# Kernel tuning notes

Measured on AMD Instinct MI355X. Metric: run time of the kernel, lower is better.

Reference implementation:

```python
import math
import jax, jax.numpy as jnp
import numpy as np


def setup_inputs() -> dict:
    key = jax.random.key(0)
    ks = jax.random.split(key, 8)
    N, Lv, M, Lt = 4096, 16, 4096, 77
    Din, D, R = 512, 768, 4  # fc in-dim, model dim, bottleneck ratio
    Dh = D // R
    s = lambda k, shape, fan_in: jax.random.normal(k, shape, jnp.float32) * (1.0 / math.sqrt(fan_in))
    return {
        "vision_prompt": jax.random.normal(ks[0], (N, Lv, D), jnp.float32),
        "text_prompt": jax.random.normal(ks[1], (M, Lt, Din), jnp.float32),
        "fc_w": s(ks[2], (D, Din), Din),        # torch Linear layout [out, in]
        "fc_b": jnp.zeros((D,), jnp.float32),
        "ln_g": jnp.ones((D,), jnp.float32),
        "ln_b": jnp.zeros((D,), jnp.float32),
        "mlp_w1": s(ks[3], (Dh, D), D),
        "mlp_b1": jnp.zeros((Dh,), jnp.float32),
        "mlp_w2": s(ks[4], (D, Dh), Dh),
        "mlp_b2": jnp.zeros((D,), jnp.float32),
    }


def _layernorm(x, g, b, eps=1e-5):
    mu = jnp.mean(x, axis=-1, keepdims=True)
    var = jnp.var(x, axis=-1, keepdims=True)
    return (x - mu) * jax.lax.rsqrt(var + eps) * g + b


def reference(vision_prompt, text_prompt, fc_w, fc_b, ln_g, ln_b,
              mlp_w1, mlp_b1, mlp_w2, mlp_b2):
    N, Lv, D = vision_prompt.shape
    mean_v = jnp.mean(vision_prompt, axis=1)                    # [N, D]
    mean_t = jnp.mean(text_prompt, axis=1)                      # [M, Din]
    t = mean_t @ fc_w.T + fc_b                                  # [M, D]
    scores = jnp.einsum('nc,mc->nm', mean_v, t) / math.sqrt(D)  # [N, M]
    aff = jax.nn.softmax(scores, axis=-1)
    agg = jnp.einsum('nm,mc->nc', aff, t)                       # [N, D]
    h = _layernorm(agg, ln_g, ln_b)
    h = jax.nn.relu(h @ mlp_w1.T + mlp_b1)
    h = h @ mlp_w2.T + mlp_b2                                   # [N, D]
    return jnp.broadcast_to(h[:, None, :], (N, Lv, D))
```

## Files before the change

kernel.cpp:

```cpp
#include <hip/hip_runtime.h>
#include <math.h>

typedef unsigned short u16;
typedef __attribute__((ext_vector_type(4))) float f32x4;
typedef __attribute__((ext_vector_type(8))) short bf16x8;

#define GLOBAL_AS __attribute__((address_space(1)))
#define LDS_AS __attribute__((address_space(3)))

__device__ __forceinline__ u16 f2bf(float f) {
  unsigned u = __builtin_bit_cast(unsigned, f);
  unsigned lsb = (u >> 16) & 1u;
  u += 0x7fffu + lsb;
  return (u16)(u >> 16);
}

__device__ __forceinline__ float bf2f(u16 b) {
  return __builtin_bit_cast(float, ((unsigned)b) << 16);
}

__device__ __forceinline__ void gload16(const void* g, void* l) {
  __builtin_amdgcn_global_load_lds((const GLOBAL_AS void*)g, (LDS_AS void*)l, 16, 0, 0);
}

__global__ __launch_bounds__(256) void prologue_kernel(
    const float* __restrict__ vision, const float* __restrict__ text,
    const float* __restrict__ fc_w, const float* __restrict__ w1,
    const float* __restrict__ w2, const float* __restrict__ b1,
    u16* __restrict__ mean_v, u16* __restrict__ mean_t,
    u16* __restrict__ fcw_bf, u16* __restrict__ w1p, u16* __restrict__ w2p,
    float* __restrict__ b1p)
{
  const int n_mv = 4096 * 192;
  const int n_mt = 4096 * 128;
  const int n_fcw = 768 * 512;
  const int n_w1 = 256 * 768;
  const int n_w2 = 768 * 256;
  int id = blockIdx.x * 256 + threadIdx.x;

  if (id < n_mv) {
    int n = id / 192, c = id % 192;
    const f32x4* x = (const f32x4*)vision + (size_t)n * 16 * 192 + c;
    f32x4 s = {0.f, 0.f, 0.f, 0.f};
#pragma unroll
    for (int l = 0; l < 16; ++l) s += x[(size_t)l * 192];
    s *= (1.f / 16.f);
    ushort4 o; o.x = f2bf(s.x); o.y = f2bf(s.y); o.z = f2bf(s.z); o.w = f2bf(s.w);
    ((ushort4*)mean_v)[id] = o;
    return;
  }
  id -= n_mv;
  if (id < n_mt) {
    int n = id / 128, c = id % 128;
    const f32x4* x = (const f32x4*)text + (size_t)n * 77 * 128 + c;
    f32x4 s = {0.f, 0.f, 0.f, 0.f};
    for (int l = 0; l < 77; ++l) s += x[(size_t)l * 128];
    s *= (1.f / 77.f);
    ushort4 o; o.x = f2bf(s.x); o.y = f2bf(s.y); o.z = f2bf(s.z); o.w = f2bf(s.w);
    ((ushort4*)mean_t)[id] = o;
    return;
  }
  id -= n_mt;
  if (id < n_fcw) { fcw_bf[id] = f2bf(fc_w[id]); return; }
  id -= n_fcw;
  if (id < n_w1) {
    int r = id / 768;
    w1p[id] = (r < 192) ? f2bf(w1[id]) : (u16)0;
    return;
  }
  id -= n_w1;
  if (id < n_w2) {
    int r = id / 256, c = id % 256;
    w2p[id] = (c < 192) ? f2bf(w2[(size_t)r * 192 + c]) : (u16)0;
    return;
  }
  id -= n_w2;
  if (id < 256) b1p[id] = (id < 192) ? b1[id] : 0.f;
}

template<bool EXP>
__global__ __launch_bounds__(512, 2) void gemm256_nt_bf16(
    const u16* __restrict__ A, const u16* __restrict__ B, float alpha,
    u16* __restrict__ C, int N, int K, int lda, int ldb)
{
  __shared__ u16 lA[3][256 * 32];
  __shared__ u16 lB[3][256 * 32];
  const int tid = threadIdx.x;
  const int w = tid >> 6, lane = tid & 63;
  const int brow = blockIdx.y * 256, bcol = blockIdx.x * 256;
  const int wr = w >> 2, wc = w & 3;

  f32x4 acc[8][4];
#pragma unroll
  for (int i = 0; i < 8; ++i)
#pragma unroll
    for (int j = 0; j < 4; ++j) acc[i][j] = (f32x4){0.f, 0.f, 0.f, 0.f};

  const int srow = lane >> 2;
  const int scol = (lane & 3) * 8;
  const size_t ga0 = (size_t)(brow + (w * 2 + 0) * 16 + srow) * lda + scol;
  const size_t ga1 = (size_t)(brow + (w * 2 + 1) * 16 + srow) * lda + scol;
  const size_t gb0 = (size_t)(bcol + (w * 2 + 0) * 16 + srow) * ldb + scol;
  const size_t gb1 = (size_t)(bcol + (w * 2 + 1) * 16 + srow) * ldb + scol;

  const int fr = lane & 15, fk = (lane >> 4) * 8;
  const int NT = K >> 5;

  auto stage = [&](int ti, int b) {
    const int k0 = ti << 5;
    char* la = (char*)&lA[b][0] + w * 2048;
    char* lb = (char*)&lB[b][0] + w * 2048;
    gload16(A + ga0 + k0, la);
    gload16(A + ga1 + k0, la + 1024);
    gload16(B + gb0 + k0, lb);
    gload16(B + gb1 + k0, lb + 1024);
  };

  stage(0, 0);
  stage(1, 1);

  int bR = 0;
  for (int it = 0; it < NT; ++it) {
    if (it + 1 < NT) { asm volatile("s_waitcnt vmcnt(4)" ::: "memory"); }
    else             { asm volatile("s_waitcnt vmcnt(0)" ::: "memory"); }
    __builtin_amdgcn_s_barrier();
    asm volatile("" ::: "memory");

    int bW = bR + 2; if (bW >= 3) bW -= 3;
    if (it + 2 < NT) stage(it + 2, bW);

    const u16* la = lA[bR];
    const u16* lb = lB[bR];
    bf16x8 av[8], bv[4];
#pragma unroll
    for (int mi = 0; mi < 8; ++mi)
      av[mi] = *(const bf16x8*)&la[(wr * 128 + mi * 16 + fr) * 32 + fk];
#pragma unroll
    for (int ni = 0; ni < 4; ++ni)
      bv[ni] = *(const bf16x8*)&lb[(wc * 64 + ni * 16 + fr) * 32 + fk];

    __builtin_amdgcn_s_setprio(1);
#pragma unroll
    for (int mi = 0; mi < 8; ++mi)
#pragma unroll
      for (int ni = 0; ni < 4; ++ni)
        acc[mi][ni] = __builtin_amdgcn_mfma_f32_16x16x32_bf16(av[mi], bv[ni], acc[mi][ni], 0, 0, 0);
    __builtin_amdgcn_s_setprio(0);

    bR = (bR + 1 == 3) ? 0 : bR + 1;
  }

  const int fq = lane >> 4;
#pragma unroll
  for (int mi = 0; mi < 8; ++mi) {
#pragma unroll
    for (int ni = 0; ni < 4; ++ni) {
      int col = bcol + wc * 64 + ni * 16 + fr;
#pragma unroll
      for (int r = 0; r < 4; ++r) {
        int row = brow + wr * 128 + mi * 16 + fq * 4 + r;
        float v = acc[mi][ni][r] * alpha;
        if (EXP) v = __expf(v);
        C[(size_t)row * N + col] = f2bf(v);
      }
    }
  }
}

template<bool RELU, bool BF16OUT>
__global__ __launch_bounds__(256) void gemm_nt(
    const u16* __restrict__ A, const u16* __restrict__ B,
    const float* __restrict__ bias, float alpha,
    float* __restrict__ Cf, u16* __restrict__ Cb,
    int M, int N, int K, int lda, int ldb,
    int kofs, long long cofs)
{
  __shared__ u16 lA[3][128 * 32];
  __shared__ u16 lB[3][128 * 32];
  const int t = threadIdx.x;
  const int w = t >> 6, lane = t & 63;
  const int brow = blockIdx.y * 128, bcol = blockIdx.x * 128;
  const int wr = w >> 1, wc = w & 1;
  const int kz = blockIdx.z;

  A += (size_t)kz * kofs;
  B += (size_t)kz * kofs;
  Cf += kz * cofs;

  f32x4 acc[4][4];
#pragma unroll
  for (int i = 0; i < 4; ++i)
#pragma unroll
    for (int j = 0; j < 4; ++j) acc[i][j] = (f32x4){0.f, 0.f, 0.f, 0.f};

  const int srow = t >> 2;
  const int scol = (t & 3) * 8;
  const size_t aoff0 = (size_t)(brow + srow) * lda + scol;
  const size_t boff0 = (size_t)(bcol + srow) * ldb + scol;
  const size_t aoff1 = aoff0 + (size_t)64 * lda;
  const size_t boff1 = boff0 + (size_t)64 * ldb;

  const int fr = lane & 15, fk = (lane >> 4) * 8;
  const int NT = K >> 5;

  auto stage = [&](int ti, int b) {
    const int k0 = ti << 5;
    char* la = (char*)&lA[b][0] + w * 1024;
    char* lb = (char*)&lB[b][0] + w * 1024;
    gload16(A + aoff0 + k0, la);
    gload16(A + aoff1 + k0, la + 4096);
    gload16(B + boff0 + k0, lb);
    gload16(B + boff1 + k0, lb + 4096);
  };

  stage(0, 0);
  stage(1, 1);

  int bR = 0;
  for (int it = 0; it < NT; ++it) {
    if (it + 1 < NT) { asm volatile("s_waitcnt vmcnt(4)" ::: "memory"); }
    else             { asm volatile("s_waitcnt vmcnt(0)" ::: "memory"); }
    __builtin_amdgcn_s_barrier();
    asm volatile("" ::: "memory");

    int bW = bR + 2; if (bW >= 3) bW -= 3;
    if (it + 2 < NT) stage(it + 2, bW);

    const u16* la = lA[bR];
    const u16* lb = lB[bR];
    bf16x8 av[4], bv[4];
#pragma unroll
    for (int mi = 0; mi < 4; ++mi)
      av[mi] = *(const bf16x8*)&la[(wr * 64 + mi * 16 + fr) * 32 + fk];
#pragma unroll
    for (int ni = 0; ni < 4; ++ni)
      bv[ni] = *(const bf16x8*)&lb[(wc * 64 + ni * 16 + fr) * 32 + fk];

    __builtin_amdgcn_s_setprio(1);
#pragma unroll
    for (int mi = 0; mi < 4; ++mi)
#pragma unroll
      for (int ni = 0; ni < 4; ++ni)
        acc[mi][ni] = __builtin_amdgcn_mfma_f32_16x16x32_bf16(av[mi], bv[ni], acc[mi][ni], 0, 0, 0);
    __builtin_amdgcn_s_setprio(0);

    bR = (bR + 1 == 3) ? 0 : bR + 1;
  }

  const int fq = lane >> 4;
#pragma unroll
  for (int mi = 0; mi < 4; ++mi) {
#pragma unroll
    for (int ni = 0; ni < 4; ++ni) {
      int col = bcol + wc * 64 + ni * 16 + fr;
      float bb = bias ? bias[col] : 0.f;
#pragma unroll
      for (int r = 0; r < 4; ++r) {
        int row = brow + wr * 64 + mi * 16 + fq * 4 + r;
        float v = acc[mi][ni][r] * alpha + bb;
        if (RELU) v = fmaxf(v, 0.f);
        if (BF16OUT) Cb[(size_t)row * N + col] = f2bf(v);
        else         Cf[(size_t)row * N + col] = v;
      }
    }
  }
}

__global__ __launch_bounds__(256) void transpose_bf16_kernel(
    const u16* __restrict__ X, u16* __restrict__ Y, int R, int C)
{
  __shared__ u16 tile[32][33];
  int bx = blockIdx.x, by = blockIdx.y;
  int tx = threadIdx.x & 31, ty = threadIdx.x >> 5;
#pragma unroll
  for (int i = 0; i < 4; ++i) {
    int r = by * 32 + ty + i * 8, c = bx * 32 + tx;
    tile[ty + i * 8][tx] = X[(size_t)r * C + c];
  }
  __syncthreads();
#pragma unroll
  for (int i = 0; i < 4; ++i) {
    int r = bx * 32 + ty + i * 8;
    int c = by * 32 + tx;
    Y[(size_t)r * R + c] = tile[tx][ty + i * 8];
  }
}

__global__ __launch_bounds__(256) void rowsum_kernel(
    const u16* __restrict__ A, float* __restrict__ denom)
{
  __shared__ float red[4];
  int row = blockIdx.x, t = threadIdx.x;
  const u16* s = A + (size_t)row * 4096;
  bf16x8 c0 = *(const bf16x8*)&s[t * 8];
  bf16x8 c1 = *(const bf16x8*)&s[2048 + t * 8];
  float sum = 0.f;
#pragma unroll
  for (int j = 0; j < 8; ++j) sum += bf2f((u16)c0[j]) + bf2f((u16)c1[j]);
#pragma unroll
  for (int off = 32; off > 0; off >>= 1) sum += __shfl_xor(sum, off);
  if ((t & 63) == 0) red[t >> 6] = sum;
  __syncthreads();
  if (t == 0) denom[row] = red[0] + red[1] + red[2] + red[3];
}

__global__ __launch_bounds__(256) void ln4_kernel(
    const float* __restrict__ X, long long ps, const float* __restrict__ denom,
    const float* __restrict__ g, const float* __restrict__ b,
    u16* __restrict__ Y)
{
  __shared__ float red[4];
  int row = blockIdx.x, t = threadIdx.x;
  const float* x = X + (size_t)row * 768;
  float inv_d = 1.f / denom[row];
  float v0 = (x[t]       + x[ps + t]       + x[2 * ps + t]       + x[3 * ps + t]) * inv_d;
  float v1 = (x[t + 256] + x[ps + t + 256] + x[2 * ps + t + 256] + x[3 * ps + t + 256]) * inv_d;
  float v2 = (x[t + 512] + x[ps + t + 512] + x[2 * ps + t + 512] + x[3 * ps + t + 512]) * inv_d;

  float s = v0 + v1 + v2;
#pragma unroll
  for (int off = 32; off > 0; off >>= 1) s += __shfl_xor(s, off);
  if ((t & 63) == 0) red[t >> 6] = s;
  __syncthreads();
  float mu = (red[0] + red[1] + red[2] + red[3]) * (1.f / 768.f);
  __syncthreads();

  float d0 = v0 - mu, d1 = v1 - mu, d2 = v2 - mu;
  float q = d0 * d0 + d1 * d1 + d2 * d2;
#pragma unroll
  for (int off = 32; off > 0; off >>= 1) q += __shfl_xor(q, off);
  if ((t & 63) == 0) red[t >> 6] = q;
  __syncthreads();
  float var = (red[0] + red[1] + red[2] + red[3]) * (1.f / 768.f);
  float inv = rsqrtf(var + 1e-5f);

  u16* y = Y + (size_t)row * 768;
  y[t]       = f2bf(d0 * inv * g[t]       + b[t]);
  y[t + 256] = f2bf(d1 * inv * g[t + 256] + b[t + 256]);
  y[t + 512] = f2bf(d2 * inv * g[t + 512] + b[t + 512]);
}

__global__ __launch_bounds__(256) void bcast_kernel(
    const f32x4* __restrict__ H, f32x4* __restrict__ O, int total, int L, int d4)
{
  int id = blockIdx.x * 256 + threadIdx.x;
  if (id >= total) return;
  int n = id / (L * d4);
  int c = id % d4;
  O[id] = H[(size_t)n * d4 + c];
}

extern "C" void kernel_launch(void* const* d_in, const int* in_sizes, int n_in,
                              void* d_out, int out_size, void* d_ws, size_t ws_size,
                              hipStream_t stream)
{
  const float* vision = (const float*)d_in[0];
  const float* text   = (const float*)d_in[1];
  const float* fc_w   = (const float*)d_in[2];
  const float* fc_b   = (const float*)d_in[3];
  const float* ln_g   = (const float*)d_in[4];
  const float* ln_b   = (const float*)d_in[5];
  const float* w1     = (const float*)d_in[6];
  const float* b1     = (const float*)d_in[7];
  const float* w2     = (const float*)d_in[8];
  const float* b2     = (const float*)d_in[9];
  float* out = (float*)d_out;

  const int N = 4096, Lv = 16, M = 4096, Din = 512, D = 768, Dhp = 256;

  char* p = (char*)d_ws;
  auto alloc = [&](size_t bytes) { char* r = p; p += (bytes + 255) & ~(size_t)255; return r; };
  u16*   mean_v = (u16*)alloc((size_t)N * D * 2);
  u16*   mean_t = (u16*)alloc((size_t)M * Din * 2);
  u16*   fcw_bf = (u16*)alloc((size_t)D * Din * 2);
  u16*   w1p    = (u16*)alloc((size_t)Dhp * D * 2);
  u16*   w2p    = (u16*)alloc((size_t)D * Dhp * 2);
  float* b1p    = (float*)alloc((size_t)Dhp * 4);
  float* denom  = (float*)alloc((size_t)N * 4);
  u16*   t_bf   = (u16*)alloc((size_t)M * D * 2);
  u16*   tT_bf  = (u16*)alloc((size_t)D * M * 2);
  u16*   aff    = (u16*)alloc((size_t)N * M * 2);
  u16*   ln_o   = (u16*)alloc((size_t)N * D * 2);
  u16*   h1     = (u16*)alloc((size_t)N * Dhp * 2);
  float* aggp   = (float*)alloc((size_t)4 * N * D * 4);
  float* h2     = (float*)aff;

  {
    int total = 4096 * 192 + 4096 * 128 + 768 * 512 + 256 * 768 + 768 * 256 + 256;
    prologue_kernel<<<(total + 255) / 256, 256, 0, stream>>>(
        vision, text, fc_w, w1, w2, b1, mean_v, mean_t, fcw_bf, w1p, w2p, b1p);
  }

  gemm_nt<false, true><<<dim3(D / 128, M / 128), 256, 0, stream>>>(
      mean_t, fcw_bf, fc_b, 1.f, nullptr, t_bf, M, D, Din, Din, Din, 0, 0);

  transpose_bf16_kernel<<<dim3(D / 32, M / 32), 256, 0, stream>>>(t_bf, tT_bf, M, D);

  gemm256_nt_bf16<true><<<dim3(M / 256, N / 256), 512, 0, stream>>>(
      mean_v, t_bf, 1.f / sqrtf(768.f), aff, M, D, D, D);

  rowsum_kernel<<<N, 256, 0, stream>>>(aff, denom);

  gemm_nt<false, false><<<dim3(D / 128, N / 128, 4), 256, 0, stream>>>(
      aff, tT_bf, nullptr, 1.f, aggp, nullptr, N, D, M / 4, M, M,
      M / 4, (long long)N * D);

  ln4_kernel<<<N, 256, 0, stream>>>(aggp, (long long)N * D, denom, ln_g, ln_b, ln_o);

  gemm_nt<true, true><<<dim3(Dhp / 128, N / 128), 256, 0, stream>>>(
      ln_o, w1p, b1p, 1.f, nullptr, h1, N, Dhp, D, D, D, 0, 0);

  gemm_nt<false, false><<<dim3(D / 128, N / 128), 256, 0, stream>>>(
      h1, w2p, b2, 1.f, h2, nullptr, N, D, Dhp, Dhp, Dhp, 0, 0);

  int total4 = N * Lv * (D / 4);
  bcast_kernel<<<(total4 + 255) / 256, 256, 0, stream>>>(
      (const f32x4*)h2, (f32x4*)out, total4, Lv, D / 4);
}
```

Before: 385.8 us.

## Fuse softmax rowsum, transpose, and broadcast into GEMM epilogues

Computes per-block partial row sums of the exponentiated scores inside the score GEMM epilogue, which removes the separate rowsum pass over the affinity matrix. The fc GEMM writes a transposed copy through LDS, replacing the standalone transpose kernel. The final MLP GEMM writes its result directly to all 16 broadcast positions, removing the intermediate h2 buffer and the broadcast kernel. The trade-off is heavier epilogues, with scalar strided stores for the broadcast and extra LDS syncs.

```diff
diff --git a/kernel.cpp b/kernel.cpp
--- a/kernel.cpp
+++ b/kernel.cpp
@@ -78,10 +78,9 @@
   if (id < 256) b1p[id] = (id < 192) ? b1[id] : 0.f;
 }
 
-template<bool EXP>
-__global__ __launch_bounds__(512, 2) void gemm256_nt_bf16(
+__global__ __launch_bounds__(512, 2) void gemm256_exp_bf16(
     const u16* __restrict__ A, const u16* __restrict__ B, float alpha,
-    u16* __restrict__ C, int N, int K, int lda, int ldb)
+    u16* __restrict__ C, float* __restrict__ dsum, int N, int K, int lda, int ldb)
 {
   __shared__ u16 lA[3][256 * 32];
   __shared__ u16 lB[3][256 * 32];
@@ -151,6 +150,12 @@
   }
 
   const int fq = lane >> 4;
+  float rsum[8][4];
+#pragma unroll
+  for (int mi = 0; mi < 8; ++mi)
+#pragma unroll
+    for (int r = 0; r < 4; ++r) rsum[mi][r] = 0.f;
+
 #pragma unroll
   for (int mi = 0; mi < 8; ++mi) {
 #pragma unroll
@@ -159,24 +164,47 @@
 #pragma unroll
       for (int r = 0; r < 4; ++r) {
         int row = brow + wr * 128 + mi * 16 + fq * 4 + r;
-        float v = acc[mi][ni][r] * alpha;
-        if (EXP) v = __expf(v);
+        float v = __expf(acc[mi][ni][r] * alpha);
         C[(size_t)row * N + col] = f2bf(v);
+        rsum[mi][r] += v;
       }
     }
   }
-}
-
-template<bool RELU, bool BF16OUT>
+#pragma unroll
+  for (int mi = 0; mi < 8; ++mi)
+#pragma unroll
+    for (int r = 0; r < 4; ++r) {
+      float s = rsum[mi][r];
+      s += __shfl_xor(s, 1); s += __shfl_xor(s, 2);
+      s += __shfl_xor(s, 4); s += __shfl_xor(s, 8);
+      rsum[mi][r] = s;
+    }
+  __syncthreads();
+  float* wsum = (float*)&lA[0][0];
+  if (fr == 0) {
+#pragma unroll
+    for (int mi = 0; mi < 8; ++mi)
+#pragma unroll
+      for (int r = 0; r < 4; ++r)
+        wsum[wc * 256 + wr * 128 + mi * 16 + fq * 4 + r] = rsum[mi][r];
+  }
+  __syncthreads();
+  if (tid < 256) {
+    float s = wsum[tid] + wsum[256 + tid] + wsum[512 + tid] + wsum[768 + tid];
+    dsum[(size_t)(brow + tid) * 16 + blockIdx.x] = s;
+  }
+}
+
+template<bool RELU, bool BF16OUT, bool TRANST, bool BCAST16>
 __global__ __launch_bounds__(256) void gemm_nt(
     const u16* __restrict__ A, const u16* __restrict__ B,
     const float* __restrict__ bias, float alpha,
     float* __restrict__ Cf, u16* __restrict__ Cb,
+    u16* __restrict__ Ct, int ldt,
     int M, int N, int K, int lda, int ldb,
     int kofs, long long cofs)
 {
-  __shared__ u16 lA[3][128 * 32];
-  __shared__ u16 lB[3][128 * 32];
+  __shared__ char lds[49152];
   const int t = threadIdx.x;
   const int w = t >> 6, lane = t & 63;
   const int brow = blockIdx.y * 128, bcol = blockIdx.x * 128;
@@ -205,8 +233,8 @@
 
   auto stage = [&](int ti, int b) {
     const int k0 = ti << 5;
-    char* la = (char*)&lA[b][0] + w * 1024;
-    char* lb = (char*)&lB[b][0] + w * 1024;
+    char* la = lds + b * 16384 + w * 1024;
+    char* lb = lds + b * 16384 + 8192 + w * 1024;
     gload16(A + aoff0 + k0, la);
     gload16(A + aoff1 + k0, la + 4096);
     gload16(B + boff0 + k0, lb);
@@ -226,8 +254,8 @@
     int bW = bR + 2; if (bW >= 3) bW -= 3;
     if (it + 2 < NT) stage(it + 2, bW);
 
-    const u16* la = lA[bR];
-    const u16* lb = lB[bR];
+    const u16* la = (const u16*)(lds + bR * 16384);
+    const u16* lb = (const u16*)(lds + bR * 16384 + 8192);
     bf16x8 av[4], bv[4];
 #pragma unroll
     for (int mi = 0; mi < 4; ++mi)
@@ -248,71 +276,60 @@
   }
 
   const int fq = lane >> 4;
+  u16* tileT = (u16*)lds;
+  if (TRANST) __syncthreads();
+
 #pragma unroll
   for (int mi = 0; mi < 4; ++mi) {
 #pragma unroll
     for (int ni = 0; ni < 4; ++ni) {
-      int col = bcol + wc * 64 + ni * 16 + fr;
+      int cl = wc * 64 + ni * 16 + fr;
+      int col = bcol + cl;
       float bb = bias ? bias[col] : 0.f;
 #pragma unroll
       for (int r = 0; r < 4; ++r) {
-        int row = brow + wr * 64 + mi * 16 + fq * 4 + r;
+        int rl = wr * 64 + mi * 16 + fq * 4 + r;
+        int row = brow + rl;
         float v = acc[mi][ni][r] * alpha + bb;
         if (RELU) v = fmaxf(v, 0.f);
-        if (BF16OUT) Cb[(size_t)row * N + col] = f2bf(v);
-        else         Cf[(size_t)row * N + col] = v;
+        if (BF16OUT) {
+          u16 bf = f2bf(v);
+          Cb[(size_t)row * N + col] = bf;
+          if (TRANST) tileT[cl * 130 + rl] = bf;
+        } else if (BCAST16) {
+          size_t b0 = ((size_t)row * 16) * (size_t)N + col;
+#pragma unroll
+          for (int l = 0; l < 16; ++l) Cf[b0 + (size_t)l * N] = v;
+        } else {
+          Cf[(size_t)row * N + col] = v;
+        }
       }
     }
   }
-}
-
-__global__ __launch_bounds__(256) void transpose_bf16_kernel(
-    const u16* __restrict__ X, u16* __restrict__ Y, int R, int C)
-{
-  __shared__ u16 tile[32][33];
-  int bx = blockIdx.x, by = blockIdx.y;
-  int tx = threadIdx.x & 31, ty = threadIdx.x >> 5;
-#pragma unroll
-  for (int i = 0; i < 4; ++i) {
-    int r = by * 32 + ty + i * 8, c = bx * 32 + tx;
-    tile[ty + i * 8][tx] = X[(size_t)r * C + c];
-  }
-  __syncthreads();
-#pragma unroll
-  for (int i = 0; i < 4; ++i) {
-    int r = bx * 32 + ty + i * 8;
-    int c = by * 32 + tx;
-    Y[(size_t)r * R + c] = tile[tx][ty + i * 8];
-  }
-}
-
-__global__ __launch_bounds__(256) void rowsum_kernel(
-    const u16* __restrict__ A, float* __restrict__ denom)
-{
-  __shared__ float red[4];
-  int row = blockIdx.x, t = threadIdx.x;
-  const u16* s = A + (size_t)row * 4096;
-  bf16x8 c0 = *(const bf16x8*)&s[t * 8];
-  bf16x8 c1 = *(const bf16x8*)&s[2048 + t * 8];
-  float sum = 0.f;
-#pragma unroll
-  for (int j = 0; j < 8; ++j) sum += bf2f((u16)c0[j]) + bf2f((u16)c1[j]);
-#pragma unroll
-  for (int off = 32; off > 0; off >>= 1) sum += __shfl_xor(sum, off);
-  if ((t & 63) == 0) red[t >> 6] = sum;
-  __syncthreads();
-  if (t == 0) denom[row] = red[0] + red[1] + red[2] + red[3];
+
+  if (TRANST) {
+    __syncthreads();
+    int c2 = t >> 1, off = (t & 1) * 64;
+    size_t base = (size_t)(bcol + c2) * ldt + brow + off;
+#pragma unroll
+    for (int j = 0; j < 8; ++j)
+      *(bf16x8*)&Ct[base + j * 8] = *(const bf16x8*)&tileT[c2 * 130 + off + j * 8];
+  }
 }
 
 __global__ __launch_bounds__(256) void ln4_kernel(
-    const float* __restrict__ X, long long ps, const float* __restrict__ denom,
+    const float* __restrict__ X, long long ps, const float* __restrict__ dsum,
     const float* __restrict__ g, const float* __restrict__ b,
     u16* __restrict__ Y)
 {
   __shared__ float red[4];
   int row = blockIdx.x, t = threadIdx.x;
   const float* x = X + (size_t)row * 768;
-  float inv_d = 1.f / denom[row];
+  float s16 = 0.f;
+#pragma unroll
+  for (int j = 0; j < 16; ++j) s16 += dsum[(size_t)row * 16 + j];
+  float inv_d = 1.f / s16;
+
   float v0 = (x[t]       + x[ps + t]       + x[2 * ps + t]       + x[3 * ps + t]) * inv_d;
   float v1 = (x[t + 256] + x[ps + t + 256] + x[2 * ps + t + 256] + x[3 * ps + t + 256]) * inv_d;
   float v2 = (x[t + 512] + x[ps + t + 512] + x[2 * ps + t + 512] + x[3 * ps + t + 512]) * inv_d;
@@ -338,16 +355,6 @@
   y[t]       = f2bf(d0 * inv * g[t]       + b[t]);
   y[t + 256] = f2bf(d1 * inv * g[t + 256] + b[t + 256]);
   y[t + 512] = f2bf(d2 * inv * g[t + 512] + b[t + 512]);
-}
-
-__global__ __launch_bounds__(256) void bcast_kernel(
-    const f32x4* __restrict__ H, f32x4* __restrict__ O, int total, int L, int d4)
-{
-  int id = blockIdx.x * 256 + threadIdx.x;
-  if (id >= total) return;
-  int n = id / (L * d4);
-  int c = id % d4;
-  O[id] = H[(size_t)n * d4 + c];
 }
 
 extern "C" void kernel_launch(void* const* d_in, const int* in_sizes, int n_in,
@@ -366,7 +373,7 @@
   const float* b2     = (const float*)d_in[9];
   float* out = (float*)d_out;
 
-  const int N = 4096, Lv = 16, M = 4096, Din = 512, D = 768, Dhp = 256;
+  const int N = 4096, M = 4096, Din = 512, D = 768, Dhp = 256;
 
   char* p = (char*)d_ws;
   auto alloc = [&](size_t bytes) { char* r = p; p += (bytes + 255) & ~(size_t)255; return r; };
@@ -376,14 +383,13 @@
   u16*   w1p    = (u16*)alloc((size_t)Dhp * D * 2);
   u16*   w2p    = (u16*)alloc((size_t)D * Dhp * 2);
   float* b1p    = (float*)alloc((size_t)Dhp * 4);
-  float* denom  = (float*)alloc((size_t)N * 4);
+  float* dsum   = (float*)alloc((size_t)N * 16 * 4);
   u16*   t_bf   = (u16*)alloc((size_t)M * D * 2);
   u16*   tT_bf  = (u16*)alloc((size_t)D * M * 2);
   u16*   aff    = (u16*)alloc((size_t)N * M * 2);
   u16*   ln_o   = (u16*)alloc((size_t)N * D * 2);
   u16*   h1     = (u16*)alloc((size_t)N * Dhp * 2);
   float* aggp   = (float*)alloc((size_t)4 * N * D * 4);
-  float* h2     = (float*)aff;
 
   {
     int total = 4096 * 192 + 4096 * 128 + 768 * 512 + 256 * 768 + 768 * 256 + 256;
@@ -391,29 +397,21 @@
         vision, text, fc_w, w1, w2, b1, mean_v, mean_t, fcw_bf, w1p, w2p, b1p);
   }
 
-  gemm_nt<false, true><<<dim3(D / 128, M / 128), 256, 0, stream>>>(
-      mean_t, fcw_bf, fc_b, 1.f, nullptr, t_bf, M, D, Din, Din, Din, 0, 0);
-
-  transpose_bf16_kernel<<<dim3(D / 32, M / 32), 256, 0, stream>>>(t_bf, tT_bf, M, D);
-
-  gemm256_nt_bf16<true><<<dim3(M / 256, N / 256), 512, 0, stream>>>(
-      mean_v, t_bf, 1.f / sqrtf(768.f), aff, M, D, D, D);
-
-  rowsum_kernel<<<N, 256, 0, stream>>>(aff, denom);
-
-  gemm_nt<false, false><<<dim3(D / 128, N / 128, 4), 256, 0, stream>>>(
-      aff, tT_bf, nullptr, 1.f, aggp, nullptr, N, D, M / 4, M, M,
+  gemm_nt<false, true, true, false><<<dim3(D / 128, M / 128), 256, 0, stream>>>(
+      mean_t, fcw_bf, fc_b, 1.f, nullptr, t_bf, tT_bf, M, M, D, Din, Din, Din, 0, 0);
+
+  gemm256_exp_bf16<<<dim3(M / 256, N / 256), 512, 0, stream>>>(
+      mean_v, t_bf, 1.f / sqrtf(768.f), aff, dsum, M, D, D, D);
+
+  gemm_nt<false, false, false, false><<<dim3(D / 128, N / 128, 4), 256, 0, stream>>>(
+      aff, tT_bf, nullptr, 1.f, aggp, nullptr, nullptr, 0, N, D, M / 4, M, M,
       M / 4, (long long)N * D);
 
-  ln4_kernel<<<N, 256, 0, stream>>>(aggp, (long long)N * D, denom, ln_g, ln_b, ln_o);
-
-  gemm_nt<true, true><<<dim3(Dhp / 128, N / 128), 256, 0, stream>>>(
-      ln_o, w1p, b1p, 1.f, nullptr, h1, N, Dhp, D, D, D, 0, 0);
-
-  gemm_nt<false, false><<<dim3(D / 128, N / 128), 256, 0, stream>>>(
-      h1, w2p, b2, 1.f, h2, nullptr, N, D, Dhp, Dhp, Dhp, 0, 0);
-
-  int total4 = N * Lv * (D / 4);
-  bcast_kernel<<<(total4 + 255) / 256, 256, 0, stream>>>(
-      (const f32x4*)h2, (f32x4*)out, total4, Lv, D / 4);
-}
+  ln4_kernel<<<N, 256, 0, stream>>>(aggp, (long long)N * D, dsum, ln_g, ln_b, ln_o);
+
+  gemm_nt<true, true, false, false><<<dim3(Dhp / 128, N / 128), 256, 0, stream>>>(
+      ln_o, w1p, b1p, 1.f, nullptr, h1, nullptr, 0, N, Dhp, D, D, D, 0, 0);
+
+  gemm_nt<false, false, false, true><<<dim3(D / 128, N / 128), 256, 0, stream>>>(
+      h1, w2p, b2, 1.f, out, nullptr, nullptr, 0, N, D, Dhp, Dhp, Dhp, 0, 0);
+}
```

Result: no change. 385.3 us (-0.1%).
